# Kernel optimization log

Hardware: AMD Instinct MI355X
Metric: run time of the kernel (lower is better)

Reference implementation:

```python
import jax, jax.numpy as jnp
import numpy as np

D_MODEL = 1024
N_LAYER = 2
VOCAB = 50257
D_STATE = 64
D_CONV = 4
EXPAND = 2
HEADDIM = 64
D_INNER = EXPAND * D_MODEL            # 2048
NHEADS = D_INNER // HEADDIM           # 32
CONV_DIM = D_INNER + 2 * D_STATE      # x, B, C share the conv (ngroups=1)
D_PROJ = 2 * D_INNER + 2 * D_STATE + NHEADS  # z, xBC, dt
D_FF = 4 * D_MODEL
B, T = 1, 1024
EPS = 1e-5


def _layernorm(x, w):
    mu = jnp.mean(x, -1, keepdims=True)
    v = jnp.mean((x - mu) ** 2, -1, keepdims=True)
    return (x - mu) * jax.lax.rsqrt(v + EPS) * w


def _rmsnorm(x, w):
    return x * jax.lax.rsqrt(jnp.mean(x ** 2, -1, keepdims=True) + EPS) * w


def setup_inputs() -> dict:
    key = jax.random.key(0)
    ks = jax.random.split(key, 16)
    std = 0.02
    idx = jax.random.randint(ks[0], (B, T), 0, VOCAB)
    targets = jax.random.randint(ks[1], (B, T), 0, VOCAB)
    E = jax.random.normal(ks[2], (VOCAB, D_MODEL)) * std  # tied embedding / lm_head
    norm_w = jnp.ones((N_LAYER, D_MODEL))
    norm2_w = jnp.ones((N_LAYER, D_MODEL))
    norm_f_w = jnp.ones((D_MODEL,))
    in_proj_w = jax.random.normal(ks[3], (N_LAYER, D_PROJ, D_MODEL)) * std
    conv_w = jax.random.normal(ks[4], (N_LAYER, CONV_DIM, D_CONV)) / np.sqrt(D_CONV)
    conv_b = jnp.zeros((N_LAYER, CONV_DIM))
    dt = jnp.exp(jax.random.uniform(ks[5], (N_LAYER, NHEADS)) * (np.log(0.1) - np.log(1e-3)) + np.log(1e-3))
    dt_bias = dt + jnp.log(-jnp.expm1(-dt))  # inverse softplus
    A_log = jnp.log(jax.random.uniform(ks[6], (N_LAYER, NHEADS), minval=1.0, maxval=16.0))
    Dp = jnp.ones((N_LAYER, NHEADS))
    gnorm_w = jnp.ones((N_LAYER, D_INNER))
    out_proj_w = jax.random.normal(ks[7], (N_LAYER, D_MODEL, D_INNER)) * std / np.sqrt(2 * N_LAYER)
    fc1_w = jax.random.normal(ks[8], (N_LAYER, 2 * D_FF, D_MODEL)) * std
    fc2_w = jax.random.normal(ks[9], (N_LAYER, D_MODEL, D_FF)) * std / np.sqrt(2 * N_LAYER)
    return {"idx": idx, "targets": targets, "E": E, "norm_w": norm_w, "norm2_w": norm2_w,
            "in_proj_w": in_proj_w, "conv_w": conv_w, "conv_b": conv_b, "dt_bias": dt_bias,
            "A_log": A_log, "Dp": Dp, "gnorm_w": gnorm_w, "out_proj_w": out_proj_w,
            "fc1_w": fc1_w, "fc2_w": fc2_w, "norm_f_w": norm_f_w}


def _mamba2(x, Wi, cw, cb, dtb, Al, Dh, gw, Wo):
    b, l, _ = x.shape
    zxbcdt = x @ Wi.T  # [b,l,D_PROJ]
    z = zxbcdt[..., :D_INNER]
    xBC = zxbcdt[..., D_INNER:D_INNER + CONV_DIM]
    dt = zxbcdt[..., D_INNER + CONV_DIM:]  # [b,l,H]
    # depthwise causal conv1d over time
    xp = jnp.pad(xBC, ((0, 0), (D_CONV - 1, 0), (0, 0)))
    xBC = sum(xp[:, k:k + l, :] * cw[:, k] for k in range(D_CONV)) + cb
    xBC = jax.nn.silu(xBC)
    xs = xBC[..., :D_INNER].reshape(b, l, NHEADS, HEADDIM)
    Bm = xBC[..., D_INNER:D_INNER + D_STATE]  # [b,l,N] (ngroups=1)
    Cm = xBC[..., D_INNER + D_STATE:]
    dt = jax.nn.softplus(dt + dtb)            # [b,l,H]
    dA = jnp.exp(dt * (-jnp.exp(Al)))         # [b,l,H]
    tm = lambda a: jnp.moveaxis(a, 1, 0)      # time-major for scan

    def step(h, inp):
        dA_t, dt_t, x_t, B_t, C_t = inp
        h = dA_t[..., None, None] * h + jnp.einsum('bh,bhp,bn->bhpn', dt_t, x_t, B_t)
        return h, jnp.einsum('bhpn,bn->bhp', h, C_t)

    h0 = jnp.zeros((b, NHEADS, HEADDIM, D_STATE), x.dtype)
    _, ys = jax.lax.scan(step, h0, (tm(dA), tm(dt), tm(xs), tm(Bm), tm(Cm)))
    y = jnp.moveaxis(ys, 0, 1) + Dh[None, None, :, None] * xs  # skip term D*x
    y = y.reshape(b, l, D_INNER)
    y = _rmsnorm(y * jax.nn.silu(z), gw)  # gated RMSNorm
    return y @ Wo.T


def _gated_mlp(x, W1, W2):
    y = x @ W1.T
    y, g = jnp.split(y, 2, axis=-1)
    return (y * jax.nn.silu(g)) @ W2.T


def reference(idx, targets, E, norm_w, norm2_w, in_proj_w, conv_w, conv_b, dt_bias,
              A_log, Dp, gnorm_w, out_proj_w, fc1_w, fc2_w, norm_f_w):
    h = E[idx]  # [B,T,D]
    for i in range(N_LAYER):
        x = _layernorm(h, norm_w[i])
        x = _mamba2(x, in_proj_w[i], conv_w[i], conv_b[i], dt_bias[i], A_log[i],
                    Dp[i], gnorm_w[i], out_proj_w[i])
        res = x + h
        x = _layernorm(res, norm2_w[i])
        h = _gated_mlp(x, fc1_w[i], fc2_w[i]) + res
    h = _layernorm(h, norm_f_w)
    logits = h @ E.T  # tied lm_head
    logp = jax.nn.log_softmax(logits, axis=-1)
    nll = -jnp.take_along_axis(logp, targets[..., None], axis=-1)[..., 0]
    loss = jnp.mean(nll)  # no ignore_index=-1 entries present
    return logits, loss
```

## Files before the change

### kernel.cpp

```cpp
#include <hip/hip_runtime.h>
#include <cmath>

#define DMODEL  1024
#define DINNER  2048
#define NHEADS  32
#define CONVDIM 2176
#define DPROJ   4256
#define VOCAB   50257
#define NBLK_V  400
#define VOCABP  (NBLK_V * 128)
#define CLEN    32
#define NCHUNK  32

typedef float f32x4 __attribute__((ext_vector_type(4)));
typedef float f32x2 __attribute__((ext_vector_type(2)));
typedef unsigned short u16;
typedef u16 u16x4 __attribute__((ext_vector_type(4)));
typedef u16 u16x8 __attribute__((ext_vector_type(8)));
typedef __bf16 bf16x8 __attribute__((ext_vector_type(8)));

__device__ __forceinline__ u16 f2bf(float f) {
  unsigned u = __builtin_bit_cast(unsigned, f);
  u += 0x7FFFu + ((u >> 16) & 1u);
  return (u16)(u >> 16);
}
__device__ __forceinline__ float silu_f(float x) { return x / (1.f + expf(-x)); }

__device__ __forceinline__ void gload16(const u16* g, u16* l) {
  __builtin_amdgcn_global_load_lds(
      (const __attribute__((address_space(1))) void*)g,
      (__attribute__((address_space(3))) void*)l,
      16, 0, 0);
}

__global__ __launch_bounds__(256) void gemm_bf16(
    const u16* __restrict__ A, const u16* __restrict__ B,
    float* __restrict__ C, int N, int K, int kslice)
{
  __shared__ alignas(128) u16 As[3 * 4096];
  __shared__ alignas(128) u16 Bs[3 * 4096];
  const int tid = threadIdx.x;
  const int m0 = blockIdx.x << 7;
  const int n0 = blockIdx.y << 7;
  const int lane = tid & 63, wid = tid >> 6;
  const int wm = (wid >> 1) << 6, wn = (wid & 1) << 6;
  const int lr = lane & 15, kg = lane >> 4;

  const int srow = wid * 16 + (lane >> 2);
  const int scol = ((lane & 3) ^ ((lane >> 3) & 3)) << 3;
  const u16* gA = A + (size_t)(m0 + srow) * K + scol;
  const u16* gB = B + (size_t)(n0 + srow) * K + scol;

  f32x4 acc[4][4];
#pragma unroll
  for (int i = 0; i < 4; ++i)
#pragma unroll
    for (int j = 0; j < 4; ++j) acc[i][j] = (f32x4){0.f, 0.f, 0.f, 0.f};

  const int kb = blockIdx.z * kslice;
  const int nt = kslice >> 5;

  auto stage = [&](int buf, int t) {
    const int ko = kb + (t << 5);
#pragma unroll
    for (int i = 0; i < 2; ++i) {
      gload16(gA + ko + (size_t)i * 64 * K, &As[buf * 4096 + i * 2048 + wid * 512]);
      gload16(gB + ko + (size_t)i * 64 * K, &Bs[buf * 4096 + i * 2048 + wid * 512]);
    }
  };

  stage(0, 0);
  stage(1, 1);
  int b0 = 0, b1 = 1, b2 = 2;
  const int cxr = ((lr >> 1) & 3);
  for (int t = 0; t < nt; ++t) {
    if (t == nt - 1) asm volatile("s_waitcnt vmcnt(0)" ::: "memory");
    else             asm volatile("s_waitcnt vmcnt(4)" ::: "memory");
    __builtin_amdgcn_s_barrier();
    if (t + 2 < nt) stage(b2, t + 2);
    bf16x8 af[4], bfr[4];
    const int po = ((kg ^ cxr) << 3);
#pragma unroll
    for (int f = 0; f < 4; ++f) {
      af[f]  = *(const bf16x8*)&As[b0 * 4096 + (wm + f * 16 + lr) * 32 + po];
      bfr[f] = *(const bf16x8*)&Bs[b0 * 4096 + (wn + f * 16 + lr) * 32 + po];
    }
#pragma unroll
    for (int i = 0; i < 4; ++i)
#pragma unroll
      for (int j = 0; j < 4; ++j)
        acc[i][j] = __builtin_amdgcn_mfma_f32_16x16x32_bf16(af[i], bfr[j], acc[i][j], 0, 0, 0);
    int tmp = b0; b0 = b1; b1 = b2; b2 = tmp;
  }

  const int mr = (lane >> 4) << 2;
  const int nc = lane & 15;
  float* Cw = C + (gridDim.z > 1 ? (size_t)blockIdx.z * 1024 * N : 0);
#pragma unroll
  for (int i = 0; i < 4; ++i)
#pragma unroll
    for (int j = 0; j < 4; ++j) {
      int n = n0 + wn + j * 16 + nc;
      if (n < N) {
#pragma unroll
        for (int e = 0; e < 4; ++e)
          Cw[(size_t)(m0 + wm + i * 16 + mr + e) * N + n] = acc[i][j][e];
      }
    }
}

__global__ __launch_bounds__(512) void gemm256(
    const u16* __restrict__ A, const u16* __restrict__ B,
    float* __restrict__ C, int N, int K,
    float* __restrict__ lsepart, int swz, int nblk,
    u16* __restrict__ glu_out)
{
  __shared__ alignas(128) u16 As[3 * 8192];
  __shared__ alignas(128) u16 Bs[3 * 4096];
  const int tid = threadIdx.x;
  int m0, n0;
  if (swz) {
    int bid = blockIdx.x;
    m0 = ((bid >> 3) & 3) << 8;
    n0 = ((bid & 7) + ((bid >> 5) << 3)) << 7;
  } else {
    m0 = blockIdx.x << 8;
    n0 = blockIdx.y << 7;
  }
  const int lane = tid & 63, wid = tid >> 6;
  const int wm = (wid >> 1) << 6, wn = (wid & 1) << 6;
  const int lr = lane & 15, kg = lane >> 4;

  const int srow = wid * 16 + (lane >> 2);
  const int scol = ((lane & 3) ^ ((lane >> 3) & 3)) << 3;
  const u16* gA = A + (size_t)(m0 + srow) * K + scol;
  const u16* gB = B + (size_t)(n0 + srow) * K + scol;

  f32x4 acc[4][4];
#pragma unroll
  for (int i = 0; i < 4; ++i)
#pragma unroll
    for (int j = 0; j < 4; ++j) acc[i][j] = (f32x4){0.f, 0.f, 0.f, 0.f};

  const int nt = K >> 5;

  auto stage = [&](int buf, int t) {
    const int ko = t << 5;
    gload16(gA + ko,                     &As[buf * 8192 + wid * 512]);
    gload16(gA + ko + (size_t)128 * K,   &As[buf * 8192 + 4096 + wid * 512]);
    gload16(gB + ko,                     &Bs[buf * 4096 + wid * 512]);
  };

  stage(0, 0);
  stage(1, 1);
  int b0 = 0, b1 = 1, b2 = 2;
  const int cxr = ((lr >> 1) & 3);
  for (int t = 0; t < nt; ++t) {
    if (t == nt - 1) asm volatile("s_waitcnt vmcnt(0)" ::: "memory");
    else             asm volatile("s_waitcnt vmcnt(3)" ::: "memory");
    __builtin_amdgcn_s_barrier();
    if (t + 2 < nt) stage(b2, t + 2);
    bf16x8 af[4], bfr[4];
    const int po = ((kg ^ cxr) << 3);
#pragma unroll
    for (int f = 0; f < 4; ++f) {
      af[f]  = *(const bf16x8*)&As[b0 * 8192 + (wm + f * 16 + lr) * 32 + po];
      bfr[f] = *(const bf16x8*)&Bs[b0 * 4096 + (wn + f * 16 + lr) * 32 + po];
    }
#pragma unroll
    for (int i = 0; i < 4; ++i)
#pragma unroll
      for (int j = 0; j < 4; ++j)
        acc[i][j] = __builtin_amdgcn_mfma_f32_16x16x32_bf16(af[i], bfr[j], acc[i][j], 0, 0, 0);
    int tmp = b0; b0 = b1; b1 = b2; b2 = tmp;
  }

  const int mr = (lane >> 4) << 2;
  const int nc = lane & 15;

  if (glu_out) {
#pragma unroll
    for (int i = 0; i < 4; ++i)
#pragma unroll
      for (int j = 0; j < 4; ++j)
#pragma unroll
        for (int e = 0; e < 4; ++e) {
          float v = acc[i][j][e];
          float p = __shfl_xor(v, 1);
          if (!(nc & 1)) {
            int q = (n0 + wn + j * 16 + nc) >> 1;
            int row = m0 + wm + i * 16 + mr + e;
            glu_out[(size_t)row * 4096 + q] = f2bf(v * silu_f(p));
          }
        }
    return;
  }

#pragma unroll
  for (int i = 0; i < 4; ++i)
#pragma unroll
    for (int j = 0; j < 4; ++j) {
      int n = n0 + wn + j * 16 + nc;
      if (n < N) {
#pragma unroll
        for (int e = 0; e < 4; ++e)
          C[(size_t)(m0 + wm + i * 16 + mr + e) * N + n] = acc[i][j][e];
      }
    }

  if (lsepart) {
    __syncthreads();
    float* Ls = (float*)As;
#pragma unroll
    for (int i = 0; i < 4; ++i)
#pragma unroll
      for (int e = 0; e < 4; ++e) {
        float pm = -1e30f;
#pragma unroll
        for (int j = 0; j < 4; ++j) {
          int n = n0 + wn + j * 16 + nc;
          if (n < N) pm = fmaxf(pm, acc[i][j][e]);
        }
#pragma unroll
        for (int o = 1; o < 16; o <<= 1) pm = fmaxf(pm, __shfl_xor(pm, o));
        float ps = 0.f;
#pragma unroll
        for (int j = 0; j < 4; ++j) {
          int n = n0 + wn + j * 16 + nc;
          if (n < N) ps += expf(acc[i][j][e] - pm);
        }
#pragma unroll
        for (int o = 1; o < 16; o <<= 1) ps += __shfl_xor(ps, o);
        if (nc == 0) {
          int row = wm + i * 16 + mr + e;
          Ls[row * 4 + (wid & 1) * 2] = pm;
          Ls[row * 4 + (wid & 1) * 2 + 1] = ps;
        }
      }
    __syncthreads();
    if (tid < 256) {
      float pa = Ls[tid * 4], sa = Ls[tid * 4 + 1];
      float pb = Ls[tid * 4 + 2], sb = Ls[tid * 4 + 3];
      float M = fmaxf(pa, pb);
      float S = sa * expf(pa - M) + sb * expf(pb - M);
      ((f32x2*)lsepart)[(size_t)(m0 + tid) * nblk + (n0 >> 7)] = (f32x2){M, S};
    }
  }
}

__global__ void k_cvt8(const float* __restrict__ src, u16* __restrict__ dst, int n8) {
  int i = blockIdx.x * 256 + threadIdx.x;
  if (i >= n8) return;
  f32x4 a = ((const f32x4*)src)[i * 2];
  f32x4 b = ((const f32x4*)src)[i * 2 + 1];
  u16x8 o = { f2bf(a[0]), f2bf(a[1]), f2bf(a[2]), f2bf(a[3]),
              f2bf(b[0]), f2bf(b[1]), f2bf(b[2]), f2bf(b[3]) };
  ((u16x8*)dst)[i] = o;
}

__global__ void k_cvt8_pad(const float* __restrict__ src, u16* __restrict__ dst,
                           int n8, int srcN8) {
  int i = blockIdx.x * 256 + threadIdx.x;
  if (i >= n8) return;
  u16x8 o;
  if (i < srcN8) {
    f32x4 a = ((const f32x4*)src)[i * 2];
    f32x4 b = ((const f32x4*)src)[i * 2 + 1];
    o = (u16x8){ f2bf(a[0]), f2bf(a[1]), f2bf(a[2]), f2bf(a[3]),
                 f2bf(b[0]), f2bf(b[1]), f2bf(b[2]), f2bf(b[3]) };
  } else {
    o = (u16x8){0, 0, 0, 0, 0, 0, 0, 0};
  }
  ((u16x8*)dst)[i] = o;
}

__global__ void k_cvt_fc1(const float* __restrict__ src, u16* __restrict__ dst, int n8) {
  int i = blockIdx.x * 256 + threadIdx.x;
  if (i >= n8) return;
  f32x4 a = ((const f32x4*)src)[i * 2];
  f32x4 b = ((const f32x4*)src)[i * 2 + 1];
  u16x8 o = { f2bf(a[0]), f2bf(a[1]), f2bf(a[2]), f2bf(a[3]),
              f2bf(b[0]), f2bf(b[1]), f2bf(b[2]), f2bf(b[3]) };
  int R = i >> 7, col8 = i & 127;
  int layer = R >> 13, r = R & 8191;
  int dstr = (r < 4096) ? (r << 1) : (((r - 4096) << 1) | 1);
  ((u16x8*)dst)[((size_t)(layer << 13) + dstr) * 128 + col8] = o;
}

__device__ __forceinline__ void ln_write(f32x4 v, const float* __restrict__ w,
                                         u16* __restrict__ out, int t, int tid) {
  float s = v[0] + v[1] + v[2] + v[3];
  float sq = v[0]*v[0] + v[1]*v[1] + v[2]*v[2] + v[3]*v[3];
#pragma unroll
  for (int o = 32; o; o >>= 1) { s += __shfl_down(s, o); sq += __shfl_down(sq, o); }
  __shared__ float sb[4], qb[4];
  if ((tid & 63) == 0) { sb[tid >> 6] = s; qb[tid >> 6] = sq; }
  __syncthreads();
  s = sb[0] + sb[1] + sb[2] + sb[3];
  sq = qb[0] + qb[1] + qb[2] + qb[3];
  float mu = s * (1.f / 1024.f);
  float rstd = rsqrtf(sq * (1.f / 1024.f) - mu * mu + 1e-5f);
  u16x4 o;
#pragma unroll
  for (int e = 0; e < 4; ++e) o[e] = f2bf((v[e] - mu) * rstd * w[tid * 4 + e]);
  ((u16x4*)out)[t * 256 + tid] = o;
}

__global__ void k_ln_embed(const int* __restrict__ idx, const float* __restrict__ E,
                           const float* __restrict__ w, float* __restrict__ hbuf,
                           u16* __restrict__ out) {
  int t = blockIdx.x, tid = threadIdx.x;
  f32x4 v = ((const f32x4*)(E + (size_t)idx[t] * DMODEL))[tid];
  ((f32x4*)hbuf)[t * 256 + tid] = v;
  ln_write(v, w, out, t, tid);
}

__global__ void k_red_ln(const float* __restrict__ part, int S,
                         float* __restrict__ hbuf, const float* __restrict__ w,
                         u16* __restrict__ out) {
  int t = blockIdx.x, tid = threadIdx.x;
  f32x4 v = ((const f32x4*)hbuf)[t * 256 + tid];
  for (int k = 0; k < S; ++k)
    v += ((const f32x4*)part)[(size_t)k * 262144 + t * 256 + tid];
  ((f32x4*)hbuf)[t * 256 + tid] = v;
  ln_write(v, w, out, t, tid);
}

__global__ void k_convdt(const float* __restrict__ zx, const float* __restrict__ cw,
                         const float* __restrict__ cb, const float* __restrict__ dtb,
                         const float* __restrict__ alog, float* __restrict__ xbc,
                         float* __restrict__ dtsp, float* __restrict__ dag) {
  int t = blockIdx.y, x = blockIdx.x, tid = threadIdx.x;
  if (x < 8 || tid < 128) {
    int c = x * 256 + tid;
    float acc = cb[c];
#pragma unroll
    for (int k = 0; k < 4; ++k) {
      int tt = t + k - 3;
      if (tt >= 0) acc += zx[(size_t)tt * DPROJ + 2048 + c] * cw[c * 4 + k];
    }
    xbc[(size_t)t * CONVDIM + c] = silu_f(acc);
  } else if (tid < 160) {
    int hh = tid - 128;
    float raw = zx[(size_t)t * DPROJ + 4224 + hh] + dtb[hh];
    float sp = raw > 20.f ? raw : log1pf(expf(raw));
    dtsp[t * 32 + hh] = sp;
    dag[t * 32 + hh] = expf(-expf(alog[hh]) * sp);
  }
}

__global__ __launch_bounds__(256) void k_scan_local(
    const float* __restrict__ xbc, const float* __restrict__ dtsp,
    const float* __restrict__ dag, float* __restrict__ yb, float* __restrict__ Sloc,
    float* __restrict__ pref, float* __restrict__ dacum)
{
  int c = blockIdx.x, hh = blockIdx.y;
  int tid = threadIdx.x;
  int p = tid >> 2, ng = tid & 3, n0 = ng << 4;
  float st[16];
#pragma unroll
  for (int j = 0; j < 16; ++j) st[j] = 0.f;
  float P = 1.f;
  for (int s_ = 0; s_ < CLEN; ++s_) {
    int t = c * CLEN + s_;
    float dA = dag[t * 32 + hh];
    P *= dA;
    if (tid == 0) pref[t * 32 + hh] = P;
    float coef = dtsp[t * 32 + hh] * xbc[(size_t)t * CONVDIM + hh * 64 + p];
    const f32x4* B4 = (const f32x4*)&xbc[(size_t)t * CONVDIM + 2048 + n0];
    const f32x4* C4 = (const f32x4*)&xbc[(size_t)t * CONVDIM + 2112 + n0];
    float y = 0.f;
#pragma unroll
    for (int q = 0; q < 4; ++q) {
      f32x4 b = B4[q], cc = C4[q];
#pragma unroll
      for (int e = 0; e < 4; ++e) {
        int j = q * 4 + e;
        st[j] = dA * st[j] + coef * b[e];
        y += st[j] * cc[e];
      }
    }
    y += __shfl_xor(y, 1);
    y += __shfl_xor(y, 2);
    if (ng == 0) yb[(size_t)t * DINNER + hh * 64 + p] = y;
  }
  if (tid == 0) dacum[c * 32 + hh] = P;
  float* Sp = Sloc + ((size_t)(c * 32 + hh) * 64 + p) * 64 + n0;
#pragma unroll
  for (int q = 0; q < 4; ++q)
    *(f32x4*)(Sp + q * 4) = (f32x4){ st[q*4], st[q*4+1], st[q*4+2], st[q*4+3] };
}

__global__ void k_chain(const float* __restrict__ Sloc, const float* __restrict__ dacum,
                        float* __restrict__ Sin) {
  int e = blockIdx.x * 256 + threadIdx.x;
  int hh = e >> 12;
  float S = 0.f;
  for (int c = 0; c < NCHUNK; c += 8) {
    float sl[8], dd[8];
#pragma unroll
    for (int j = 0; j < 8; ++j) sl[j] = Sloc[(size_t)(c + j) * 131072 + e];
#pragma unroll
    for (int j = 0; j < 8; ++j) dd[j] = dacum[(c + j) * 32 + hh];
#pragma unroll
    for (int j = 0; j < 8; ++j) {
      Sin[(size_t)(c + j) * 131072 + e] = S;
      S = dd[j] * S + sl[j];
    }
  }
}

__global__ __launch_bounds__(256) void k_scan_fix(
    const float* __restrict__ xbc, const float* __restrict__ pref,
    const float* __restrict__ Sin, const float* __restrict__ Dp,
    float* __restrict__ yb)
{
  __shared__ float Sl[64 * 68];
  int c = blockIdx.x, hh = blockIdx.y;
  int tid = threadIdx.x;
  for (int i = 0; i < 16; ++i) {
    int e = i * 256 + tid;
    Sl[(e >> 6) * 68 + (e & 63)] = Sin[(size_t)(c * 32 + hh) * 4096 + e];
  }
  __syncthreads();
  int p = tid >> 2, ng = tid & 3, n0 = ng << 4;
  float Dh = Dp[hh];
  for (int s_ = 0; s_ < CLEN; ++s_) {
    int t = c * CLEN + s_;
    const f32x4* C4 = (const f32x4*)&xbc[(size_t)t * CONVDIM + 2112 + n0];
    float yc = 0.f;
#pragma unroll
    for (int q = 0; q < 4; ++q) {
      f32x4 cc = C4[q];
#pragma unroll
      for (int e = 0; e < 4; ++e) yc += Sl[p * 68 + n0 + q * 4 + e] * cc[e];
    }
    yc += __shfl_xor(yc, 1);
    yc += __shfl_xor(yc, 2);
    if (ng == 0) {
      size_t oy = (size_t)t * DINNER + hh * 64 + p;
      yb[oy] = yb[oy] + pref[t * 32 + hh] * yc + Dh * xbc[(size_t)t * CONVDIM + hh * 64 + p];
    }
  }
}

__global__ void k_gated_rms(const float* __restrict__ yb, const float* __restrict__ zx,
                            const float* __restrict__ gw, u16* __restrict__ out) {
  int t = blockIdx.x, tid = threadIdx.x;
  float v[8], ss = 0.f;
#pragma unroll
  for (int i = 0; i < 8; ++i) {
    int j = tid + i * 256;
    float z = zx[(size_t)t * DPROJ + j];
    float vv = yb[(size_t)t * DINNER + j] * silu_f(z);
    v[i] = vv; ss += vv * vv;
  }
#pragma unroll
  for (int o = 32; o; o >>= 1) ss += __shfl_down(ss, o);
  __shared__ float sb[4];
  if ((tid & 63) == 0) sb[tid >> 6] = ss;
  __syncthreads();
  ss = sb[0] + sb[1] + sb[2] + sb[3];
  float rstd = rsqrtf(ss * (1.f / 2048.f) + 1e-5f);
#pragma unroll
  for (int i = 0; i < 8; ++i) {
    int j = tid + i * 256;
    out[(size_t)t * DINNER + j] = f2bf(v[i] * rstd * gw[j]);
  }
}

__global__ void k_loss_final(const float* __restrict__ lsepart,
                             const float* __restrict__ logits,
                             const int* __restrict__ tgt, float* __restrict__ part) {
  int t = blockIdx.x, tid = threadIdx.x;
  float m = -1e30f, s = 0.f;
  for (int nb = tid; nb < NBLK_V; nb += 256) {
    f32x2 v = ((const f32x2*)lsepart)[(size_t)t * NBLK_V + nb];
    float M = fmaxf(m, v[0]);
    s = s * expf(m - M) + v[1] * expf(v[0] - M);
    m = M;
  }
#pragma unroll
  for (int o = 32; o; o >>= 1) {
    float m2 = __shfl_down(m, o), s2 = __shfl_down(s, o);
    float M = fmaxf(m, m2);
    s = s * expf(m - M) + s2 * expf(m2 - M);
    m = M;
  }
  __shared__ float ms[4], ssh[4];
  if ((tid & 63) == 0) { ms[tid >> 6] = m; ssh[tid >> 6] = s; }
  __syncthreads();
  if (tid == 0) {
    float M = ms[0], S = ssh[0];
    for (int w = 1; w < 4; ++w) {
      float M2 = fmaxf(M, ms[w]);
      S = S * expf(M - M2) + ssh[w] * expf(ms[w] - M2);
      M = M2;
    }
    part[t] = (M + logf(S)) - logits[(size_t)t * VOCAB + tgt[t]];
  }
}

__global__ void k_loss_mean(const float* __restrict__ part, float* __restrict__ out) {
  int tid = threadIdx.x;
  float s = 0.f;
  for (int j = tid; j < 1024; j += 256) s += part[j];
#pragma unroll
  for (int o = 32; o; o >>= 1) s += __shfl_down(s, o);
  __shared__ float sb[4];
  if ((tid & 63) == 0) sb[tid >> 6] = s;
  __syncthreads();
  if (tid == 0) out[0] = (sb[0] + sb[1] + sb[2] + sb[3]) * (1.f / 1024.f);
}

extern "C" void kernel_launch(void* const* d_in, const int* in_sizes, int n_in,
                              void* d_out, int out_size, void* d_ws, size_t ws_size,
                              hipStream_t stream)
{
  const int*   idx       = (const int*)d_in[0];
  const int*   tgt       = (const int*)d_in[1];
  const float* E         = (const float*)d_in[2];
  const float* norm_w    = (const float*)d_in[3];
  const float* norm2_w   = (const float*)d_in[4];
  const float* in_proj_w = (const float*)d_in[5];
  const float* conv_w    = (const float*)d_in[6];
  const float* conv_b    = (const float*)d_in[7];
  const float* dt_bias   = (const float*)d_in[8];
  const float* A_log     = (const float*)d_in[9];
  const float* Dp        = (const float*)d_in[10];
  const float* gnorm_w   = (const float*)d_in[11];
  const float* out_proj_w= (const float*)d_in[12];
  const float* fc1_w     = (const float*)d_in[13];
  const float* fc2_w     = (const float*)d_in[14];
  const float* norm_f_w  = (const float*)d_in[15];
  float* logits = (float*)d_out;
  (void)in_sizes; (void)n_in; (void)out_size; (void)ws_size;

  char* W = (char*)d_ws;
  size_t off = 0;
  auto A8 = [&](size_t bytes) { void* p = W + off; off = (off + bytes + 255) & ~(size_t)255; return p; };
  float* hbuf   = (float*)A8((size_t)1024 * 1024 * 4);
  u16*   xnormb = (u16*)  A8((size_t)1024 * 1024 * 2);
  u16*   gatedb = (u16*)  A8((size_t)1024 * 2048 * 2);
  u16*   glub   = (u16*)  A8((size_t)1024 * 4096 * 2);
  float* dtsp   = (float*)A8((size_t)1024 * 32 * 4);
  float* dag    = (float*)A8((size_t)1024 * 32 * 4);
  float* pref   = (float*)A8((size_t)1024 * 32 * 4);
  float* dacum  = (float*)A8((size_t)2048 * 4);
  float* lpart  = (float*)A8((size_t)1024 * 4);
  float* lsebuf = (float*)A8((size_t)1024 * NBLK_V * 2 * 4);
  u16*   wip    = (u16*)  A8((size_t)2 * 4352 * 1024 * 2);
  u16*   wop    = (u16*)  A8((size_t)2 * 1024 * 2048 * 2);
  u16*   wfc1   = (u16*)  A8((size_t)2 * 8192 * 1024 * 2);
  u16*   wfc2   = (u16*)  A8((size_t)2 * 1024 * 4096 * 2);
  char*  span   = (char*)A8((size_t)117964800);
  float* big0   = (float*)(span);
  float* xbc    = (float*)(span + 33554432);
  float* yb     = (float*)(span + 33554432 + 8912896);
  float* Sloc   = (float*)(span + 33554432 + 8912896 + 8388608);
  float* Sin    = (float*)((char*)Sloc + 33554432);
  float* part   = Sloc;
  u16*   Ebf    = (u16*)span;

  dim3 b256(256), b512(512);

  k_cvt8_pad<<<dim3((4352*1024/8 + 255)/256), b256, 0, stream>>>(
      in_proj_w, wip, 4352*1024/8, 4256*1024/8);
  k_cvt8_pad<<<dim3((4352*1024/8 + 255)/256), b256, 0, stream>>>(
      in_proj_w + (size_t)4256*1024, wip + (size_t)4352*1024, 4352*1024/8, 4256*1024/8);
  k_cvt8<<<dim3(2*1024*2048/8/256), b256, 0, stream>>>(out_proj_w, wop, 2*1024*2048/8);
  k_cvt_fc1<<<dim3(2*8192*1024/8/256), b256, 0, stream>>>(fc1_w, wfc1, 2*8192*1024/8);
  k_cvt8<<<dim3(2*1024*4096/8/256), b256, 0, stream>>>(fc2_w, wfc2, 2*1024*4096/8);

  k_ln_embed<<<1024, b256, 0, stream>>>(idx, E, norm_w, hbuf, xnormb);

  const float* nw_next[2] = { norm_w + 1024, norm_f_w };
  for (int L = 0; L < 2; ++L) {
    gemm_bf16<<<dim3(8, 34, 1), b256, 0, stream>>>(
        xnormb, wip + (size_t)L * 4352 * 1024, big0, DPROJ, 1024, 1024);
    k_convdt<<<dim3(9, 1024), b256, 0, stream>>>(
        big0, conv_w + L * CONVDIM * 4, conv_b + L * CONVDIM,
        dt_bias + L * 32, A_log + L * 32, xbc, dtsp, dag);
    k_scan_local<<<dim3(NCHUNK, 32), b256, 0, stream>>>(xbc, dtsp, dag, yb, Sloc, pref, dacum);
    k_chain<<<512, b256, 0, stream>>>(Sloc, dacum, Sin);
    k_scan_fix<<<dim3(NCHUNK, 32), b256, 0, stream>>>(xbc, pref, Sin, Dp + L * 32, yb);
    k_gated_rms<<<1024, b256, 0, stream>>>(yb, big0, gnorm_w + L * 2048, gatedb);
    gemm_bf16<<<dim3(8, 8, 4), b256, 0, stream>>>(
        gatedb, wop + (size_t)L * 1024 * 2048, part, 1024, 2048, 512);
    k_red_ln<<<1024, b256, 0, stream>>>(part, 4, hbuf, norm2_w + L * 1024, xnormb);
    gemm256<<<dim3(4, 64, 1), b512, 0, stream>>>(
        xnormb, wfc1 + (size_t)L * 8192 * 1024, nullptr, 8192, 1024,
        nullptr, 0, 64, glub);
    gemm_bf16<<<dim3(8, 8, 8), b256, 0, stream>>>(
        glub, wfc2 + (size_t)L * 1024 * 4096, part, 1024, 4096, 512);
    k_red_ln<<<1024, b256, 0, stream>>>(part, 8, hbuf, nw_next[L], xnormb);
  }

  k_cvt8_pad<<<dim3((VOCABP*1024/8 + 255)/256), b256, 0, stream>>>(
      E, Ebf, VOCABP*1024/8, VOCAB*1024/8);
  gemm256<<<dim3(4 * NBLK_V, 1, 1), b512, 0, stream>>>(
      xnormb, Ebf, logits, VOCAB, 1024, lsebuf, 1, NBLK_V, nullptr);
  k_loss_final<<<1024, b256, 0, stream>>>(lsebuf, logits, tgt, lpart);
  k_loss_mean<<<1, b256, 0, stream>>>(lpart, logits + (size_t)1024 * VOCAB);
}
```

Baseline: 786.0 us.

## Fuse fp32-to-bf16 weight conversion into GEMM B-operand loading

Removes the separate weight conversion kernels (in_proj, out_proj, fc1, fc2, and the embedding for the lm_head). The GEMMs now read fp32 weights straight from global memory into registers, round them to bf16 and write them to a double-buffered LDS tile, while the A operand keeps using direct global-to-LDS loads. The fc1 interleaving is now done by remapping rows at load time, and the GLU epilogue pairs adjacent accumulator fragments instead of shuffling. This cuts a full extra pass over roughly 260MB of weights plus the bf16 writes. In exchange, every GEMM tile rereads fp32 weights at twice the bytes, redoes the conversion per M-block, and the B stream goes through registers with tighter synchronisation.

```diff
diff --git a/kernel.cpp b/kernel.cpp
--- a/kernel.cpp
+++ b/kernel.cpp
@@ -8,7 +8,6 @@
 #define DPROJ   4256
 #define VOCAB   50257
 #define NBLK_V  400
-#define VOCABP  (NBLK_V * 128)
 #define CLEN    32
 #define NCHUNK  32
 
@@ -32,24 +31,38 @@
       (__attribute__((address_space(3))) void*)l,
       16, 0, 0);
 }
-
-__global__ __launch_bounds__(256) void gemm_bf16(
-    const u16* __restrict__ A, const u16* __restrict__ B,
+__device__ __forceinline__ void vm_wait2() { asm volatile("s_waitcnt vmcnt(2)" ::: "memory"); }
+__device__ __forceinline__ void vm_wait0() { asm volatile("s_waitcnt vmcnt(0)" ::: "memory"); }
+__device__ __forceinline__ void lgkm0()    { asm volatile("s_waitcnt lgkmcnt(0)" ::: "memory"); }
+__device__ __forceinline__ void barrier_() {
+  __builtin_amdgcn_s_barrier();
+  __builtin_amdgcn_sched_barrier(0);
+}
+
+__global__ __launch_bounds__(256) void gemm128(
+    const u16* __restrict__ A, const float* __restrict__ B,
     float* __restrict__ C, int N, int K, int kslice)
 {
   __shared__ alignas(128) u16 As[3 * 4096];
-  __shared__ alignas(128) u16 Bs[3 * 4096];
+  __shared__ alignas(128) u16 Bs[2 * 4096];
   const int tid = threadIdx.x;
   const int m0 = blockIdx.x << 7;
   const int n0 = blockIdx.y << 7;
   const int lane = tid & 63, wid = tid >> 6;
   const int wm = (wid >> 1) << 6, wn = (wid & 1) << 6;
   const int lr = lane & 15, kg = lane >> 4;
-
-  const int srow = wid * 16 + (lane >> 2);
-  const int scol = ((lane & 3) ^ ((lane >> 3) & 3)) << 3;
-  const u16* gA = A + (size_t)(m0 + srow) * K + scol;
-  const u16* gB = B + (size_t)(n0 + srow) * K + scol;
+  const int kb = blockIdx.z * kslice;
+
+  const int srowA = wid * 16 + (lane >> 2);
+  const int scolA = ((lane & 3) ^ ((lane >> 3) & 3)) << 3;
+  const u16* gA = A + (size_t)(m0 + srowA) * K + scolA;
+
+  const int brow = tid >> 1, bcp = (tid & 1) << 1;
+  const int bkey = (brow >> 1) & 3;
+  const bool bvalid = (n0 + brow) < N;
+  const float* gB = B + (size_t)(bvalid ? n0 + brow : 0) * K + kb + (bcp << 3);
+  u16* wB0 = &Bs[brow * 32 + ((bcp ^ bkey) << 3)];
+  u16* wB1 = &Bs[brow * 32 + (((bcp + 1) ^ bkey) << 3)];
 
   f32x4 acc[4][4];
 #pragma unroll
@@ -57,40 +70,55 @@
 #pragma unroll
     for (int j = 0; j < 4; ++j) acc[i][j] = (f32x4){0.f, 0.f, 0.f, 0.f};
 
-  const int kb = blockIdx.z * kslice;
   const int nt = kslice >> 5;
 
-  auto stage = [&](int buf, int t) {
+  auto stageA = [&](int buf, int t) {
     const int ko = kb + (t << 5);
-#pragma unroll
-    for (int i = 0; i < 2; ++i) {
-      gload16(gA + ko + (size_t)i * 64 * K, &As[buf * 4096 + i * 2048 + wid * 512]);
-      gload16(gB + ko + (size_t)i * 64 * K, &Bs[buf * 4096 + i * 2048 + wid * 512]);
-    }
+    gload16(gA + ko,                    &As[buf * 4096 + wid * 512]);
+    gload16(gA + ko + (size_t)64 * K,   &As[buf * 4096 + 2048 + wid * 512]);
   };
-
-  stage(0, 0);
-  stage(1, 1);
-  int b0 = 0, b1 = 1, b2 = 2;
-  const int cxr = ((lr >> 1) & 3);
+  f32x4 r0, r1, r2, r3;
+  auto loadB = [&](int t) {
+    const float* p = gB + (t << 5);
+    r0 = *(const f32x4*)(p);     r1 = *(const f32x4*)(p + 4);
+    r2 = *(const f32x4*)(p + 8); r3 = *(const f32x4*)(p + 12);
+  };
+  auto writeB = [&](int t) {
+    u16x8 o0, o1;
+#pragma unroll
+    for (int e = 0; e < 4; ++e) {
+      o0[e] = bvalid ? f2bf(r0[e]) : (u16)0; o0[4+e] = bvalid ? f2bf(r1[e]) : (u16)0;
+      o1[e] = bvalid ? f2bf(r2[e]) : (u16)0; o1[4+e] = bvalid ? f2bf(r3[e]) : (u16)0;
+    }
+    *(u16x8*)(wB0 + (t & 1) * 4096) = o0;
+    *(u16x8*)(wB1 + (t & 1) * 4096) = o1;
+  };
+
+  loadB(0); stageA(0, 0); stageA(1, 1);
+  vm_wait2();
+  writeB(0); lgkm0(); barrier_();
+
+  const int cxr = (lr >> 1) & 3;
   for (int t = 0; t < nt; ++t) {
-    if (t == nt - 1) asm volatile("s_waitcnt vmcnt(0)" ::: "memory");
-    else             asm volatile("s_waitcnt vmcnt(4)" ::: "memory");
-    __builtin_amdgcn_s_barrier();
-    if (t + 2 < nt) stage(b2, t + 2);
+    if (t + 1 < nt) loadB(t + 1);
+    if (t + 2 < nt) stageA((t + 2) % 3, t + 2);
     bf16x8 af[4], bfr[4];
-    const int po = ((kg ^ cxr) << 3);
+    const int po = (kg ^ cxr) << 3;
+    const int ab = (t % 3) * 4096, bb = (t & 1) * 4096;
 #pragma unroll
     for (int f = 0; f < 4; ++f) {
-      af[f]  = *(const bf16x8*)&As[b0 * 4096 + (wm + f * 16 + lr) * 32 + po];
-      bfr[f] = *(const bf16x8*)&Bs[b0 * 4096 + (wn + f * 16 + lr) * 32 + po];
+      af[f]  = *(const bf16x8*)&As[ab + (wm + f * 16 + lr) * 32 + po];
+      bfr[f] = *(const bf16x8*)&Bs[bb + (wn + f * 16 + lr) * 32 + po];
     }
 #pragma unroll
     for (int i = 0; i < 4; ++i)
 #pragma unroll
       for (int j = 0; j < 4; ++j)
         acc[i][j] = __builtin_amdgcn_mfma_f32_16x16x32_bf16(af[i], bfr[j], acc[i][j], 0, 0, 0);
-    int tmp = b0; b0 = b1; b1 = b2; b2 = tmp;
+    if (t + 1 < nt) {
+      if (t + 2 < nt) vm_wait2(); else vm_wait0();
+      writeB(t + 1); lgkm0(); barrier_();
+    }
   }
 
   const int mr = (lane >> 4) << 2;
@@ -110,13 +138,13 @@
 }
 
 __global__ __launch_bounds__(512) void gemm256(
-    const u16* __restrict__ A, const u16* __restrict__ B,
+    const u16* __restrict__ A, const float* __restrict__ B,
     float* __restrict__ C, int N, int K,
     float* __restrict__ lsepart, int swz, int nblk,
-    u16* __restrict__ glu_out)
+    u16* __restrict__ glu_out, int fc1mode)
 {
   __shared__ alignas(128) u16 As[3 * 8192];
-  __shared__ alignas(128) u16 Bs[3 * 4096];
+  __shared__ alignas(128) u16 Bs[2 * 4096];
   const int tid = threadIdx.x;
   int m0, n0;
   if (swz) {
@@ -131,10 +159,19 @@
   const int wm = (wid >> 1) << 6, wn = (wid & 1) << 6;
   const int lr = lane & 15, kg = lane >> 4;
 
-  const int srow = wid * 16 + (lane >> 2);
-  const int scol = ((lane & 3) ^ ((lane >> 3) & 3)) << 3;
-  const u16* gA = A + (size_t)(m0 + srow) * K + scol;
-  const u16* gB = B + (size_t)(n0 + srow) * K + scol;
+  const int srowA = wid * 16 + (lane >> 2);
+  const int scolA = ((lane & 3) ^ ((lane >> 3) & 3)) << 3;
+  const u16* gA = A + (size_t)(m0 + srowA) * K + scolA;
+
+  const int brow = tid >> 2, bchunk = tid & 3;
+  int bsrc;
+  if (fc1mode) {
+    int s = brow >> 4, inner = brow & 15;
+    bsrc = ((s & 1) << 12) + (n0 >> 1) + ((s >> 1) << 4) + inner;
+  } else bsrc = n0 + brow;
+  const bool bvalid = bsrc < N;
+  const float* gB = B + (size_t)(bvalid ? bsrc : 0) * K + (bchunk << 3);
+  u16* wB0 = &Bs[brow * 32 + ((bchunk ^ ((brow >> 1) & 3)) << 3)];
 
   f32x4 acc[4][4];
 #pragma unroll
@@ -144,35 +181,51 @@
 
   const int nt = K >> 5;
 
-  auto stage = [&](int buf, int t) {
+  auto stageA = [&](int buf, int t) {
     const int ko = t << 5;
-    gload16(gA + ko,                     &As[buf * 8192 + wid * 512]);
-    gload16(gA + ko + (size_t)128 * K,   &As[buf * 8192 + 4096 + wid * 512]);
-    gload16(gB + ko,                     &Bs[buf * 4096 + wid * 512]);
+    gload16(gA + ko,                    &As[buf * 8192 + wid * 512]);
+    gload16(gA + ko + (size_t)128 * K,  &As[buf * 8192 + 4096 + wid * 512]);
   };
-
-  stage(0, 0);
-  stage(1, 1);
-  int b0 = 0, b1 = 1, b2 = 2;
-  const int cxr = ((lr >> 1) & 3);
+  f32x4 r0, r1;
+  auto loadB = [&](int t) {
+    const float* p = gB + (t << 5);
+    r0 = *(const f32x4*)(p); r1 = *(const f32x4*)(p + 4);
+  };
+  auto writeB = [&](int t) {
+    u16x8 o;
+#pragma unroll
+    for (int e = 0; e < 4; ++e) {
+      o[e]     = bvalid ? f2bf(r0[e]) : (u16)0;
+      o[4 + e] = bvalid ? f2bf(r1[e]) : (u16)0;
+    }
+    *(u16x8*)(wB0 + (t & 1) * 4096) = o;
+  };
+
+  loadB(0); stageA(0, 0); stageA(1, 1);
+  vm_wait2();
+  writeB(0); lgkm0(); barrier_();
+
+  const int cxr = (lr >> 1) & 3;
   for (int t = 0; t < nt; ++t) {
-    if (t == nt - 1) asm volatile("s_waitcnt vmcnt(0)" ::: "memory");
-    else             asm volatile("s_waitcnt vmcnt(3)" ::: "memory");
-    __builtin_amdgcn_s_barrier();
-    if (t + 2 < nt) stage(b2, t + 2);
+    if (t + 1 < nt) loadB(t + 1);
+    if (t + 2 < nt) stageA((t + 2) % 3, t + 2);
     bf16x8 af[4], bfr[4];
-    const int po = ((kg ^ cxr) << 3);
+    const int po = (kg ^ cxr) << 3;
+    const int ab = (t % 3) * 8192, bb = (t & 1) * 4096;
 #pragma unroll
     for (int f = 0; f < 4; ++f) {
-      af[f]  = *(const bf16x8*)&As[b0 * 8192 + (wm + f * 16 + lr) * 32 + po];
-      bfr[f] = *(const bf16x8*)&Bs[b0 * 4096 + (wn + f * 16 + lr) * 32 + po];
+      af[f]  = *(const bf16x8*)&As[ab + (wm + f * 16 + lr) * 32 + po];
+      bfr[f] = *(const bf16x8*)&Bs[bb + (wn + f * 16 + lr) * 32 + po];
     }
 #pragma unroll
     for (int i = 0; i < 4; ++i)
 #pragma unroll
       for (int j = 0; j < 4; ++j)
         acc[i][j] = __builtin_amdgcn_mfma_f32_16x16x32_bf16(af[i], bfr[j], acc[i][j], 0, 0, 0);
-    int tmp = b0; b0 = b1; b1 = b2; b2 = tmp;
+    if (t + 1 < nt) {
+      if (t + 2 < nt) vm_wait2(); else vm_wait0();
+      writeB(t + 1); lgkm0(); barrier_();
+    }
   }
 
   const int mr = (lane >> 4) << 2;
@@ -182,16 +235,13 @@
 #pragma unroll
     for (int i = 0; i < 4; ++i)
 #pragma unroll
-      for (int j = 0; j < 4; ++j)
+      for (int j = 0; j < 4; j += 2)
 #pragma unroll
         for (int e = 0; e < 4; ++e) {
-          float v = acc[i][j][e];
-          float p = __shfl_xor(v, 1);
-          if (!(nc & 1)) {
-            int q = (n0 + wn + j * 16 + nc) >> 1;
-            int row = m0 + wm + i * 16 + mr + e;
-            glu_out[(size_t)row * 4096 + q] = f2bf(v * silu_f(p));
-          }
+          float y = acc[i][j][e], g = acc[i][j + 1][e];
+          int q = (n0 >> 1) + (wn >> 1) + ((j >> 1) << 4) + nc;
+          int row = m0 + wm + i * 16 + mr + e;
+          glu_out[(size_t)row * 4096 + q] = f2bf(y * silu_f(g));
         }
     return;
   }
@@ -246,45 +296,6 @@
       ((f32x2*)lsepart)[(size_t)(m0 + tid) * nblk + (n0 >> 7)] = (f32x2){M, S};
     }
   }
-}
-
-__global__ void k_cvt8(const float* __restrict__ src, u16* __restrict__ dst, int n8) {
-  int i = blockIdx.x * 256 + threadIdx.x;
-  if (i >= n8) return;
-  f32x4 a = ((const f32x4*)src)[i * 2];
-  f32x4 b = ((const f32x4*)src)[i * 2 + 1];
-  u16x8 o = { f2bf(a[0]), f2bf(a[1]), f2bf(a[2]), f2bf(a[3]),
-              f2bf(b[0]), f2bf(b[1]), f2bf(b[2]), f2bf(b[3]) };
-  ((u16x8*)dst)[i] = o;
-}
-
-__global__ void k_cvt8_pad(const float* __restrict__ src, u16* __restrict__ dst,
-                           int n8, int srcN8) {
-  int i = blockIdx.x * 256 + threadIdx.x;
-  if (i >= n8) return;
-  u16x8 o;
-  if (i < srcN8) {
-    f32x4 a = ((const f32x4*)src)[i * 2];
-    f32x4 b = ((const f32x4*)src)[i * 2 + 1];
-    o = (u16x8){ f2bf(a[0]), f2bf(a[1]), f2bf(a[2]), f2bf(a[3]),
-                 f2bf(b[0]), f2bf(b[1]), f2bf(b[2]), f2bf(b[3]) };
-  } else {
-    o = (u16x8){0, 0, 0, 0, 0, 0, 0, 0};
-  }
-  ((u16x8*)dst)[i] = o;
-}
-
-__global__ void k_cvt_fc1(const float* __restrict__ src, u16* __restrict__ dst, int n8) {
-  int i = blockIdx.x * 256 + threadIdx.x;
-  if (i >= n8) return;
-  f32x4 a = ((const f32x4*)src)[i * 2];
-  f32x4 b = ((const f32x4*)src)[i * 2 + 1];
-  u16x8 o = { f2bf(a[0]), f2bf(a[1]), f2bf(a[2]), f2bf(a[3]),
-              f2bf(b[0]), f2bf(b[1]), f2bf(b[2]), f2bf(b[3]) };
-  int R = i >> 7, col8 = i & 127;
-  int layer = R >> 13, r = R & 8191;
-  int dstr = (r < 4096) ? (r << 1) : (((r - 4096) << 1) | 1);
-  ((u16x8*)dst)[((size_t)(layer << 13) + dstr) * 128 + col8] = o;
 }
 
 __device__ __forceinline__ void ln_write(f32x4 v, const float* __restrict__ w,
@@ -549,35 +560,21 @@
   float* dacum  = (float*)A8((size_t)2048 * 4);
   float* lpart  = (float*)A8((size_t)1024 * 4);
   float* lsebuf = (float*)A8((size_t)1024 * NBLK_V * 2 * 4);
-  u16*   wip    = (u16*)  A8((size_t)2 * 4352 * 1024 * 2);
-  u16*   wop    = (u16*)  A8((size_t)2 * 1024 * 2048 * 2);
-  u16*   wfc1   = (u16*)  A8((size_t)2 * 8192 * 1024 * 2);
-  u16*   wfc2   = (u16*)  A8((size_t)2 * 1024 * 4096 * 2);
-  char*  span   = (char*)A8((size_t)117964800);
-  float* big0   = (float*)(span);
-  float* xbc    = (float*)(span + 33554432);
-  float* yb     = (float*)(span + 33554432 + 8912896);
-  float* Sloc   = (float*)(span + 33554432 + 8912896 + 8388608);
-  float* Sin    = (float*)((char*)Sloc + 33554432);
+  float* big0   = (float*)A8((size_t)1024 * DPROJ * 4);
+  float* xbc    = (float*)A8((size_t)1024 * CONVDIM * 4);
+  float* yb     = (float*)A8((size_t)1024 * DINNER * 4);
+  float* Sloc   = (float*)A8((size_t)32 * 1024 * 1024);
+  float* Sin    = (float*)A8((size_t)16 * 1024 * 1024);
   float* part   = Sloc;
-  u16*   Ebf    = (u16*)span;
 
   dim3 b256(256), b512(512);
-
-  k_cvt8_pad<<<dim3((4352*1024/8 + 255)/256), b256, 0, stream>>>(
-      in_proj_w, wip, 4352*1024/8, 4256*1024/8);
-  k_cvt8_pad<<<dim3((4352*1024/8 + 255)/256), b256, 0, stream>>>(
-      in_proj_w + (size_t)4256*1024, wip + (size_t)4352*1024, 4352*1024/8, 4256*1024/8);
-  k_cvt8<<<dim3(2*1024*2048/8/256), b256, 0, stream>>>(out_proj_w, wop, 2*1024*2048/8);
-  k_cvt_fc1<<<dim3(2*8192*1024/8/256), b256, 0, stream>>>(fc1_w, wfc1, 2*8192*1024/8);
-  k_cvt8<<<dim3(2*1024*4096/8/256), b256, 0, stream>>>(fc2_w, wfc2, 2*1024*4096/8);
 
   k_ln_embed<<<1024, b256, 0, stream>>>(idx, E, norm_w, hbuf, xnormb);
 
   const float* nw_next[2] = { norm_w + 1024, norm_f_w };
   for (int L = 0; L < 2; ++L) {
-    gemm_bf16<<<dim3(8, 34, 1), b256, 0, stream>>>(
-        xnormb, wip + (size_t)L * 4352 * 1024, big0, DPROJ, 1024, 1024);
+    gemm128<<<dim3(8, 34, 1), b256, 0, stream>>>(
+        xnormb, in_proj_w + (size_t)L * DPROJ * 1024, big0, DPROJ, 1024, 1024);
     k_convdt<<<dim3(9, 1024), b256, 0, stream>>>(
         big0, conv_w + L * CONVDIM * 4, conv_b + L * CONVDIM,
         dt_bias + L * 32, A_log + L * 32, xbc, dtsp, dag);
@@ -585,21 +582,19 @@
     k_chain<<<512, b256, 0, stream>>>(Sloc, dacum, Sin);
     k_scan_fix<<<dim3(NCHUNK, 32), b256, 0, stream>>>(xbc, pref, Sin, Dp + L * 32, yb);
     k_gated_rms<<<1024, b256, 0, stream>>>(yb, big0, gnorm_w + L * 2048, gatedb);
-    gemm_bf16<<<dim3(8, 8, 4), b256, 0, stream>>>(
-        gatedb, wop + (size_t)L * 1024 * 2048, part, 1024, 2048, 512);
+    gemm128<<<dim3(8, 8, 4), b256, 0, stream>>>(
+        gatedb, out_proj_w + (size_t)L * 1024 * 2048, part, 1024, 2048, 512);
     k_red_ln<<<1024, b256, 0, stream>>>(part, 4, hbuf, norm2_w + L * 1024, xnormb);
     gemm256<<<dim3(4, 64, 1), b512, 0, stream>>>(
-        xnormb, wfc1 + (size_t)L * 8192 * 1024, nullptr, 8192, 1024,
-        nullptr, 0, 64, glub);
-    gemm_bf16<<<dim3(8, 8, 8), b256, 0, stream>>>(
-        glub, wfc2 + (size_t)L * 1024 * 4096, part, 1024, 4096, 512);
+        xnormb, fc1_w + (size_t)L * 8192 * 1024, nullptr, 8192, 1024,
+        nullptr, 0, 64, glub, 1);
+    gemm128<<<dim3(8, 8, 8), b256, 0, stream>>>(
+        glub, fc2_w + (size_t)L * 1024 * 4096, part, 1024, 4096, 512);
     k_red_ln<<<1024, b256, 0, stream>>>(part, 8, hbuf, nw_next[L], xnormb);
   }
 
-  k_cvt8_pad<<<dim3((VOCABP*1024/8 + 255)/256), b256, 0, stream>>>(
-      E, Ebf, VOCABP*1024/8, VOCAB*1024/8);
   gemm256<<<dim3(4 * NBLK_V, 1, 1), b512, 0, stream>>>(
-      xnormb, Ebf, logits, VOCAB, 1024, lsebuf, 1, NBLK_V, nullptr);
+      xnormb, E, logits, VOCAB, 1024, lsebuf, 1, NBLK_V, nullptr, 0);
   k_loss_final<<<1024, b256, 0, stream>>>(lsebuf, logits, tgt, lpart);
   k_loss_mean<<<1, b256, 0, stream>>>(lpart, logits + (size_t)1024 * VOCAB);
 }
```

Measured after the change: 846.7 us. 7.7% more time.
